# Optimization experiments

Measured on AMD Instinct MI355X. Metric: run time of the kernel, lower is better.

Reference implementation:

```python
import jax, jax.numpy as jnp
import numpy as np

N, E, F_IN, H = 100000, 500000, 1433, 32


def setup_inputs() -> dict:
    key = jax.random.key(0)
    ks = jax.random.split(key, 8)
    return {
        "x": jax.random.normal(ks[0], (N, F_IN), jnp.float32),
        "edge_index": jax.random.randint(ks[1], (2, E), 0, N, dtype=jnp.int32),
        "W1l": jax.random.normal(ks[2], (H, F_IN), jnp.float32) * 0.02,
        "b1l": jnp.zeros((H,), jnp.float32),
        "W1r": jax.random.normal(ks[3], (H, F_IN), jnp.float32) * 0.02,
        "W2l": jax.random.normal(ks[4], (H, H), jnp.float32) * 0.1,
        "b2l": jnp.zeros((H,), jnp.float32),
        "W2r": jax.random.normal(ks[5], (H, H), jnp.float32) * 0.1,
    }


def _sage_conv(x, src, tgt, Wl, bl, Wr, n_nodes):
    # PyG SAGEConv (mean aggr): out = lin_l(mean_{j->i} x_j) + lin_r(x_i)
    msg_sum = jax.ops.segment_sum(x[src], tgt, num_segments=n_nodes)  # [N, d]
    cnt = jax.ops.segment_sum(jnp.ones((src.shape[0],), x.dtype), tgt,
                              num_segments=n_nodes)                  # [N]
    agg = msg_sum / jnp.maximum(cnt, 1.0)[:, None]  # isolated nodes -> 0
    return agg @ Wl.T + bl + x @ Wr.T


def reference(x, edge_index, W1l, b1l, W1r, W2l, b2l, W2r):
    src, tgt = edge_index[0], edge_index[1]
    n = x.shape[0]
    h = _sage_conv(x, src, tgt, W1l, b1l, W1r, n)   # [N, 32]
    h = _sage_conv(h, src, tgt, W2l, b2l, W2r, n)   # [N, 32]
    h = jax.nn.relu(h)
    # dropout is identity in eval mode (training=False)
    return jax.nn.log_softmax(h, axis=1)
```

## Files before the change

### kernel.cpp

```cpp
#include <hip/hip_runtime.h>
#include <hip/hip_bf16.h>


typedef __attribute__((ext_vector_type(8))) __bf16 bf16x8;
typedef __attribute__((ext_vector_type(4))) float f32x4;

constexpr int K1 = 1433;
constexpr int KP1 = 1536;
constexpr int BK = 32;
constexpr int NS = 45;
constexpr int BM = 128;
constexpr int CONV_BLOCKS = (64 * KP1 + 64 * 32 + 255) / 256;

__device__ __forceinline__ void gload_lds16(const void* g, void* l) {
  __builtin_amdgcn_global_load_lds(
      reinterpret_cast<const __attribute__((address_space(1))) void*>(
          reinterpret_cast<uintptr_t>(g)),
      reinterpret_cast<__attribute__((address_space(3))) void*>(
          reinterpret_cast<uintptr_t>(l)),
      16, 0, 0);
}

__device__ __forceinline__ bf16x8 cvt8(const float4 lo, const float4 hi) {
  bf16x8 r;
  r[0] = (__bf16)lo.x; r[1] = (__bf16)lo.y;
  r[2] = (__bf16)lo.z; r[3] = (__bf16)lo.w;
  r[4] = (__bf16)hi.x; r[5] = (__bf16)hi.y;
  r[6] = (__bf16)hi.z; r[7] = (__bf16)hi.w;
  return r;
}

__global__ __launch_bounds__(256) void conv_zero(
    const float* __restrict__ W1l, const float* __restrict__ W1r,
    const float* __restrict__ W2l, const float* __restrict__ W2r,
    __bf16* __restrict__ wb1, __bf16* __restrict__ wb2,
    int* __restrict__ zbuf, int zcount) {
  if ((int)blockIdx.x < CONV_BLOCKS) {
    const int t = blockIdx.x * 256 + threadIdx.x;
    if (t < 64 * KP1) {
      const int c = t / KP1, k = t - c * KP1;
      float v = 0.0f;
      if (k < K1)
        v = (c < 32) ? W1l[(long)c * K1 + k] : W1r[(long)(c - 32) * K1 + k];
      wb1[t] = (__bf16)v;
    } else {
      const int u = t - 64 * KP1;
      if (u < 64 * 32) {
        const int c = u >> 5, k = u & 31;
        const float v = (c < 32) ? W2l[c * 32 + k] : W2r[(c - 32) * 32 + k];
        wb2[u] = (__bf16)v;
      }
    }
  } else {
    const int base = (blockIdx.x - CONV_BLOCKS) * 4096 + threadIdx.x * 16;
#pragma unroll
    for (int j = 0; j < 16; ++j) {
      const int i = base + j;
      if (i < zcount) zbuf[i] = 0;
    }
  }
}

__global__ __launch_bounds__(256) void gemm_big(const float* __restrict__ X,
                                                const __bf16* __restrict__ WB,
                                                __bf16* __restrict__ yl,
                                                float* __restrict__ yr,
                                                int Nrows, int gemmBlocks,
                                                const int* __restrict__ ei,
                                                int* __restrict__ deg, int E) {
  __shared__ float ldsA[2][BM][BK];
  __shared__ __bf16 ldsB[2][64][BK];
  if ((int)blockIdx.x >= gemmBlocks) {
    const int base = ((int)blockIdx.x - gemmBlocks) * 1024 + threadIdx.x;
#pragma unroll
    for (int j = 0; j < 4; ++j) {
      const int e = base + j * 256;
      if (e < E) atomicAdd(&deg[ei[E + e]], 1);
    }
    return;
  }
  const int tid = threadIdx.x;
  const int w = tid >> 6, l = tid & 63;
  const int lr = l & 15, lg = l >> 4;
  const int row0 = blockIdx.x * BM;

  const int aRowIn = (l >> 3);
  const int aChunk = (l & 7) ^ aRowIn;
  long aRow[4];
#pragma unroll
  for (int i = 0; i < 4; ++i) {
    long r = (long)row0 + w * 32 + i * 8 + aRowIn;
    if (r >= Nrows) r = Nrows - 1;
    aRow[i] = r;
  }
  const float* const pAmax = X + (size_t)Nrows * K1 - 4;
  const int bRow = w * 16 + (l >> 2);
  const int bChunk = (l & 3) ^ ((l >> 3) & 3);
  const __bf16* const pB0 = WB + (long)bRow * KP1 + bChunk * 8;

  auto stage = [&](int s, int buf) {
    const int k0 = s * BK;
#pragma unroll
    for (int i = 0; i < 4; ++i) {
      const float* g = X + aRow[i] * K1 + k0 + aChunk * 4;
      if (g > pAmax) g = pAmax;
      gload_lds16(g, &ldsA[buf][w * 32 + i * 8][0]);
    }
    gload_lds16(pB0 + k0, &ldsB[buf][w * 16][0]);
  };

  f32x4 acc[2][4];
#pragma unroll
  for (int t = 0; t < 2; ++t)
#pragma unroll
    for (int j = 0; j < 4; ++j) acc[t][j] = (f32x4){0.f, 0.f, 0.f, 0.f};

  const int swzA = lr & 7;
  const int swzB = (lr >> 1) & 3;

  stage(0, 0);
#pragma unroll 1
  for (int s = 0; s < NS; ++s) {
    const int buf = s & 1;
    if (s + 1 < NS) {
      stage(s + 1, buf ^ 1);
      asm volatile("s_waitcnt vmcnt(5)" ::: "memory");
    } else {
      asm volatile("s_waitcnt vmcnt(0)" ::: "memory");
    }
    __builtin_amdgcn_s_barrier();
    __builtin_amdgcn_sched_barrier(0);
    bf16x8 bfrag[4];
#pragma unroll
    for (int ct = 0; ct < 4; ++ct) {
      const int br = ct * 16 + lr;
      bfrag[ct] = *reinterpret_cast<const bf16x8*>(
          &ldsB[buf][br][(lg ^ swzB) * 8]);
    }
#pragma unroll
    for (int t = 0; t < 2; ++t) {
      const int fr = w * 32 + t * 16 + lr;
      const float4 u = *reinterpret_cast<const float4*>(
          &ldsA[buf][fr][((lg * 2 + 0) ^ swzA) * 4]);
      const float4 v = *reinterpret_cast<const float4*>(
          &ldsA[buf][fr][((lg * 2 + 1) ^ swzA) * 4]);
      const bf16x8 af = cvt8(u, v);
#pragma unroll
      for (int ct = 0; ct < 4; ++ct)
        acc[t][ct] =
            __builtin_amdgcn_mfma_f32_16x16x32_bf16(af, bfrag[ct], acc[t][ct], 0, 0, 0);
    }
    __builtin_amdgcn_sched_barrier(0);
    __builtin_amdgcn_s_barrier();
  }

#pragma unroll
  for (int t = 0; t < 2; ++t) {
#pragma unroll
    for (int j = 0; j < 4; ++j) {
      const long R = (long)row0 + w * 32 + t * 16 + lg * 4 + j;
      if (R < Nrows) {
#pragma unroll
        for (int ct = 0; ct < 2; ++ct)
          yl[R * 32 + ct * 16 + lr] = (__bf16)acc[t][ct][j];
#pragma unroll
        for (int ct = 2; ct < 4; ++ct)
          yr[R * 32 + (ct - 2) * 16 + lr] = acc[t][ct][j];
      }
    }
  }
}

__global__ __launch_bounds__(256) void csr_scan(const int* __restrict__ deg,
                                                int* __restrict__ tileSum,
                                                int* __restrict__ cnt,
                                                int* __restrict__ off, int n,
                                                int nT) {
  __shared__ int warpTot[4];
  __shared__ int tileOffS;
  const int b = blockIdx.x, t = threadIdx.x;
  const int base = b * 2048 + t * 8;
  int v[8];
  int s = 0;
#pragma unroll
  for (int j = 0; j < 8; ++j) {
    const int i = base + j;
    v[j] = (i < n) ? deg[i] : 0;
    s += v[j];
  }
  const int l = t & 63, w = t >> 6;
  int inc = s;
#pragma unroll
  for (int d = 1; d < 64; d <<= 1) {
    const int o = __shfl_up(inc, d);
    if (l >= d) inc += o;
  }
  if (l == 63) warpTot[w] = inc;
  __syncthreads();
  const int blockTot = warpTot[0] + warpTot[1] + warpTot[2] + warpTot[3];
  int wo = 0;
  for (int k = 0; k < w; ++k) wo += warpTot[k];
  if (t == 0) {
    __hip_atomic_store(&tileSum[b], blockTot, __ATOMIC_RELEASE,
                       __HIP_MEMORY_SCOPE_AGENT);
    atomicAdd(cnt, 1);
    while (__hip_atomic_load(cnt, __ATOMIC_ACQUIRE,
                             __HIP_MEMORY_SCOPE_AGENT) < nT) {
    }
  }
  __syncthreads();
  int tv = 0;
  if (t < 64) {
    int x2 = (t < b) ? __hip_atomic_load(&tileSum[t], __ATOMIC_ACQUIRE,
                                         __HIP_MEMORY_SCOPE_AGENT)
                     : 0;
#pragma unroll
    for (int d = 1; d < 64; d <<= 1) x2 += __shfl_xor(x2, d);
    tv = x2;
  }
  if (t == 0) tileOffS = tv;
  __syncthreads();
  int ex = tileOffS + wo + (inc - s);
#pragma unroll
  for (int j = 0; j < 8; ++j) {
    const int i = base + j;
    if (i < n) {
      off[i] = ex;
      ex += v[j];
    }
  }
}

__global__ __launch_bounds__(256) void scatter_src(const int* __restrict__ ei,
                                                   const int* __restrict__ off,
                                                   int* __restrict__ fill,
                                                   int* __restrict__ ssrc,
                                                   int E) {
  const int e = blockIdx.x * 256 + threadIdx.x;
  if (e < E) {
    const int t = ei[E + e];
    const int p = off[t] + atomicAdd(&fill[t], 1);
    ssrc[p] = ei[e];
  }
}

__global__ __launch_bounds__(256) void agg_gemm2(
    const int* __restrict__ off, const int* __restrict__ deg,
    const int* __restrict__ ssrc, const __bf16* __restrict__ yl1,
    const float* __restrict__ yr1, const float* __restrict__ b1,
    const __bf16* __restrict__ WB2, __bf16* __restrict__ yl2,
    float* __restrict__ yr2, int N) {
  __shared__ __bf16 hs[64][40];
  const int tid = threadIdx.x;
  const int nb0 = blockIdx.x * 64;
  const int c = tid & 31, r8 = tid >> 5;

  int stA[8], dgA[8];
#pragma unroll
  for (int j = 0; j < 8; ++j) {
    const int i = nb0 + r8 * 8 + j;
    stA[j] = (i < N) ? off[i] : 0;
    dgA[j] = (i < N) ? deg[i] : 0;
  }
#pragma unroll 1
  for (int j = 0; j < 8; ++j) {
    const int i = nb0 + r8 * 8 + j;
    float hv = 0.0f;
    if (i < N) {
      const int st = stA[j], d = dgA[j];
      float acc = 0.0f;
      int e = 0;
      for (; e + 4 <= d; e += 4) {
        const int s0 = ssrc[st + e + 0];
        const int s1 = ssrc[st + e + 1];
        const int s2 = ssrc[st + e + 2];
        const int s3 = ssrc[st + e + 3];
        acc += (float)yl1[(long)s0 * 32 + c] + (float)yl1[(long)s1 * 32 + c] +
               (float)yl1[(long)s2 * 32 + c] + (float)yl1[(long)s3 * 32 + c];
      }
      for (; e < d; ++e) acc += (float)yl1[(long)ssrc[st + e] * 32 + c];
      hv = acc / fmaxf((float)d, 1.0f) + b1[c] + yr1[(long)i * 32 + c];
    }
    hs[r8 * 8 + j][c] = (__bf16)hv;
  }
  __syncthreads();

  const int w = tid >> 6, l = tid & 63;
  const int lr = l & 15, lg = l >> 4;
  const bf16x8 af = *reinterpret_cast<const bf16x8*>(&hs[w * 16 + lr][lg * 8]);
  f32x4 acc4[4];
#pragma unroll
  for (int j = 0; j < 4; ++j) acc4[j] = (f32x4){0.f, 0.f, 0.f, 0.f};
#pragma unroll
  for (int ct = 0; ct < 4; ++ct) {
    const bf16x8 bf = *reinterpret_cast<const bf16x8*>(
        WB2 + (ct * 16 + lr) * 32 + lg * 8);
    acc4[ct] = __builtin_amdgcn_mfma_f32_16x16x32_bf16(af, bf, acc4[ct], 0, 0, 0);
  }
#pragma unroll
  for (int j = 0; j < 4; ++j) {
    const long R = (long)nb0 + w * 16 + lg * 4 + j;
    if (R < N) {
#pragma unroll
      for (int ct = 0; ct < 2; ++ct)
        yl2[R * 32 + ct * 16 + lr] = (__bf16)acc4[ct][j];
#pragma unroll
      for (int ct = 2; ct < 4; ++ct)
        yr2[R * 32 + (ct - 2) * 16 + lr] = acc4[ct][j];
    }
  }
}

__global__ __launch_bounds__(256) void agg_final(
    const int* __restrict__ off, const int* __restrict__ deg,
    const int* __restrict__ ssrc, const __bf16* __restrict__ yl2,
    const float* __restrict__ yr2, const float* __restrict__ bias,
    float* __restrict__ out, int N) {
  const int t = blockIdx.x * 256 + threadIdx.x;
  const int i = t >> 5, c = t & 31;
  if (i >= N) return;
  const int st = off[i], d = deg[i];
  float acc = 0.0f;
  int e = 0;
  for (; e + 4 <= d; e += 4) {
    const int s0 = ssrc[st + e + 0];
    const int s1 = ssrc[st + e + 1];
    const int s2 = ssrc[st + e + 2];
    const int s3 = ssrc[st + e + 3];
    acc += (float)yl2[(long)s0 * 32 + c] + (float)yl2[(long)s1 * 32 + c] +
           (float)yl2[(long)s2 * 32 + c] + (float)yl2[(long)s3 * 32 + c];
  }
  for (; e < d; ++e) acc += (float)yl2[(long)ssrc[st + e] * 32 + c];
  const float mean = acc / fmaxf((float)d, 1.0f);
  float v = mean + bias[c] + yr2[(long)i * 32 + c];
  v = fmaxf(v, 0.0f);
  float m = v;
#pragma unroll
  for (int dd = 16; dd >= 1; dd >>= 1) m = fmaxf(m, __shfl_xor(m, dd));
  const float ex = __expf(v - m);
  float s = ex;
#pragma unroll
  for (int dd = 16; dd >= 1; dd >>= 1) s += __shfl_xor(s, dd);
  out[(long)i * 32 + c] = (v - m) - __logf(s);
}

extern "C" void kernel_launch(void* const* d_in, const int* in_sizes, int n_in,
                              void* d_out, int out_size, void* d_ws,
                              size_t ws_size, hipStream_t stream) {
  const float* x = (const float*)d_in[0];
  const int* ei = (const int*)d_in[1];
  const float* W1l = (const float*)d_in[2];
  const float* b1l = (const float*)d_in[3];
  const float* W1r = (const float*)d_in[4];
  const float* W2l = (const float*)d_in[5];
  const float* b2l = (const float*)d_in[6];
  const float* W2r = (const float*)d_in[7];
  float* out = (float*)d_out;

  const int N = in_sizes[0] / K1;
  const int E = in_sizes[1] / 2;
  const int nTiles = (N + 2047) / 2048;

  char* ws = (char*)d_ws;
  size_t o = 0;
  auto alloc = [&](size_t bytes) {
    void* p = ws + o;
    o += (bytes + 255) & ~(size_t)255;
    return p;
  };
  __bf16* yl1 = (__bf16*)alloc((size_t)N * 32 * 2);
  float* yr1 = (float*)alloc((size_t)N * 32 * 4);
  __bf16* yl2 = (__bf16*)alloc((size_t)N * 32 * 2);
  float* yr2 = (float*)alloc((size_t)N * 32 * 4);
  __bf16* wb1 = (__bf16*)alloc((size_t)64 * KP1 * 2);
  __bf16* wb2 = (__bf16*)alloc((size_t)64 * 32 * 2);
  int* deg = (int*)alloc((size_t)(2 * N + 64) * 4);
  int* fill = deg + N;
  int* cnt = deg + 2 * N;
  int* off = (int*)alloc((size_t)N * 4);
  int* ssrc = (int*)alloc((size_t)E * 4);
  int* tileSum = (int*)alloc(64 * 4);

  const int zcount = 2 * N + 64;
  const int zBlocks = (zcount + 4095) / 4096;
  conv_zero<<<CONV_BLOCKS + zBlocks, 256, 0, stream>>>(W1l, W1r, W2l, W2r,
                                                       wb1, wb2, deg, zcount);
  const int gemmBlocks = (N + BM - 1) / BM;
  const int histBlocks = (E + 1023) / 1024;
  gemm_big<<<gemmBlocks + histBlocks, 256, 0, stream>>>(
      x, wb1, yl1, yr1, N, gemmBlocks, ei, deg, E);
  csr_scan<<<nTiles, 256, 0, stream>>>(deg, tileSum, cnt, off, N, nTiles);
  scatter_src<<<(E + 255) / 256, 256, 0, stream>>>(ei, off, fill, ssrc, E);
  agg_gemm2<<<(N + 63) / 64, 256, 0, stream>>>(off, deg, ssrc, yl1, yr1, b1l,
                                               wb2, yl2, yr2, N);
  agg_final<<<(N * 32 + 255) / 256, 256, 0, stream>>>(off, deg, ssrc, yl2,
                                                      yr2, b2l, out, N);
}
```

Before: 265.6 us.

## Fuse degree histogram, CSR scan and scatter into the big GEMM launch

Folds the edge histogram, the prefix scan over node degrees and the source scatter into role blocks at the front of the layer-1 GEMM launch. The stages are ordered by atomic counters with spin-waits, so CSR construction overlaps the dense GEMM and two kernel launches go away. The risks are deadlock or stalls if the role blocks are not all co-resident, and role blocks holding compute units the GEMM could otherwise use. Because the role blocks have the lowest block IDs they are likely dispatched first.

```diff
diff --git a/kernel.cpp b/kernel.cpp
--- a/kernel.cpp
+++ b/kernel.cpp
@@ -11,6 +11,8 @@
 constexpr int NS = 45;
 constexpr int BM = 128;
 constexpr int CONV_BLOCKS = (64 * KP1 + 64 * 32 + 255) / 256;
+constexpr int HIST_BLOCKS = 192;
+constexpr int SCAT_BLOCKS = 128;
 
 __device__ __forceinline__ void gload_lds16(const void* g, void* l) {
   __builtin_amdgcn_global_load_lds(
@@ -61,28 +63,113 @@
   }
 }
 
-__global__ __launch_bounds__(256) void gemm_big(const float* __restrict__ X,
-                                                const __bf16* __restrict__ WB,
-                                                __bf16* __restrict__ yl,
-                                                float* __restrict__ yr,
-                                                int Nrows, int gemmBlocks,
-                                                const int* __restrict__ ei,
-                                                int* __restrict__ deg, int E) {
+__global__ __launch_bounds__(256) void gemm_fused(
+    const float* __restrict__ X, const __bf16* __restrict__ WB,
+    __bf16* __restrict__ yl, float* __restrict__ yr, int Nrows,
+    const int* __restrict__ ei, int* __restrict__ deg, int E,
+    int* __restrict__ off, int* __restrict__ fill, int* __restrict__ ssrc,
+    int* __restrict__ tileSum, int* __restrict__ cnts, int nT) {
   __shared__ float ldsA[2][BM][BK];
   __shared__ __bf16 ldsB[2][64][BK];
-  if ((int)blockIdx.x >= gemmBlocks) {
-    const int base = ((int)blockIdx.x - gemmBlocks) * 1024 + threadIdx.x;
-#pragma unroll
-    for (int j = 0; j < 4; ++j) {
-      const int e = base + j * 256;
-      if (e < E) atomicAdd(&deg[ei[E + e]], 1);
-    }
+  __shared__ int warpTot[4];
+  __shared__ int tileOffS;
+  const int bid = blockIdx.x;
+  const int tid = threadIdx.x;
+  const int roleEnd = HIST_BLOCKS + nT + SCAT_BLOCKS;
+
+  if (bid < HIST_BLOCKS) {
+    for (int e = bid * 256 + tid; e < E; e += HIST_BLOCKS * 256)
+      atomicAdd(&deg[ei[E + e]], 1);
+    __threadfence();
+    __syncthreads();
+    if (tid == 0) atomicAdd(&cnts[0], 1);
     return;
   }
-  const int tid = threadIdx.x;
+  if (bid < HIST_BLOCKS + nT) {
+    const int b = bid - HIST_BLOCKS;
+    if (tid == 0) {
+      while (__hip_atomic_load(&cnts[0], __ATOMIC_ACQUIRE,
+                               __HIP_MEMORY_SCOPE_AGENT) < HIST_BLOCKS) {
+        __builtin_amdgcn_s_sleep(2);
+      }
+    }
+    __syncthreads();
+    const int base = b * 2048 + tid * 8;
+    int v[8];
+    int s = 0;
+#pragma unroll
+    for (int j = 0; j < 8; ++j) {
+      const int i = base + j;
+      v[j] = (i < Nrows) ? deg[i] : 0;
+      s += v[j];
+    }
+    const int l = tid & 63, w = tid >> 6;
+    int inc = s;
+#pragma unroll
+    for (int d = 1; d < 64; d <<= 1) {
+      const int o = __shfl_up(inc, d);
+      if (l >= d) inc += o;
+    }
+    if (l == 63) warpTot[w] = inc;
+    __syncthreads();
+    const int blockTot = warpTot[0] + warpTot[1] + warpTot[2] + warpTot[3];
+    int wo = 0;
+    for (int k = 0; k < w; ++k) wo += warpTot[k];
+    if (tid == 0) {
+      __hip_atomic_store(&tileSum[b], blockTot, __ATOMIC_RELEASE,
+                         __HIP_MEMORY_SCOPE_AGENT);
+      atomicAdd(&cnts[1], 1);
+      while (__hip_atomic_load(&cnts[1], __ATOMIC_ACQUIRE,
+                               __HIP_MEMORY_SCOPE_AGENT) < nT) {
+        __builtin_amdgcn_s_sleep(2);
+      }
+    }
+    __syncthreads();
+    int tv = 0;
+    if (tid < 64) {
+      int x2 = (tid < b) ? __hip_atomic_load(&tileSum[tid], __ATOMIC_ACQUIRE,
+                                             __HIP_MEMORY_SCOPE_AGENT)
+                         : 0;
+#pragma unroll
+      for (int d = 1; d < 64; d <<= 1) x2 += __shfl_xor(x2, d);
+      tv = x2;
+    }
+    if (tid == 0) tileOffS = tv;
+    __syncthreads();
+    int ex = tileOffS + wo + (inc - s);
+#pragma unroll
+    for (int j = 0; j < 8; ++j) {
+      const int i = base + j;
+      if (i < Nrows) {
+        off[i] = ex;
+        ex += v[j];
+      }
+    }
+    __threadfence();
+    __syncthreads();
+    if (tid == 0) atomicAdd(&cnts[2], 1);
+    return;
+  }
+  if (bid < roleEnd) {
+    if (tid == 0) {
+      while (__hip_atomic_load(&cnts[2], __ATOMIC_ACQUIRE,
+                               __HIP_MEMORY_SCOPE_AGENT) < nT) {
+        __builtin_amdgcn_s_sleep(2);
+      }
+    }
+    __syncthreads();
+    const int sb = bid - HIST_BLOCKS - nT;
+    for (int e = sb * 256 + tid; e < E; e += SCAT_BLOCKS * 256) {
+      const int t = ei[E + e];
+      const int p = off[t] + atomicAdd(&fill[t], 1);
+      ssrc[p] = ei[e];
+    }
+    return;
+  }
+
   const int w = tid >> 6, l = tid & 63;
   const int lr = l & 15, lg = l >> 4;
-  const int row0 = blockIdx.x * BM;
+  const int row0 = (bid - roleEnd) * BM;
 
   const int aRowIn = (l >> 3);
   const int aChunk = (l & 7) ^ aRowIn;
@@ -168,79 +255,6 @@
           yr[R * 32 + (ct - 2) * 16 + lr] = acc[t][ct][j];
       }
     }
-  }
-}
-
-__global__ __launch_bounds__(256) void csr_scan(const int* __restrict__ deg,
-                                                int* __restrict__ tileSum,
-                                                int* __restrict__ cnt,
-                                                int* __restrict__ off, int n,
-                                                int nT) {
-  __shared__ int warpTot[4];
-  __shared__ int tileOffS;
-  const int b = blockIdx.x, t = threadIdx.x;
-  const int base = b * 2048 + t * 8;
-  int v[8];
-  int s = 0;
-#pragma unroll
-  for (int j = 0; j < 8; ++j) {
-    const int i = base + j;
-    v[j] = (i < n) ? deg[i] : 0;
-    s += v[j];
-  }
-  const int l = t & 63, w = t >> 6;
-  int inc = s;
-#pragma unroll
-  for (int d = 1; d < 64; d <<= 1) {
-    const int o = __shfl_up(inc, d);
-    if (l >= d) inc += o;
-  }
-  if (l == 63) warpTot[w] = inc;
-  __syncthreads();
-  const int blockTot = warpTot[0] + warpTot[1] + warpTot[2] + warpTot[3];
-  int wo = 0;
-  for (int k = 0; k < w; ++k) wo += warpTot[k];
-  if (t == 0) {
-    __hip_atomic_store(&tileSum[b], blockTot, __ATOMIC_RELEASE,
-                       __HIP_MEMORY_SCOPE_AGENT);
-    atomicAdd(cnt, 1);
-    while (__hip_atomic_load(cnt, __ATOMIC_ACQUIRE,
-                             __HIP_MEMORY_SCOPE_AGENT) < nT) {
-    }
-  }
-  __syncthreads();
-  int tv = 0;
-  if (t < 64) {
-    int x2 = (t < b) ? __hip_atomic_load(&tileSum[t], __ATOMIC_ACQUIRE,
-                                         __HIP_MEMORY_SCOPE_AGENT)
-                     : 0;
-#pragma unroll
-    for (int d = 1; d < 64; d <<= 1) x2 += __shfl_xor(x2, d);
-    tv = x2;
-  }
-  if (t == 0) tileOffS = tv;
-  __syncthreads();
-  int ex = tileOffS + wo + (inc - s);
-#pragma unroll
-  for (int j = 0; j < 8; ++j) {
-    const int i = base + j;
-    if (i < n) {
-      off[i] = ex;
-      ex += v[j];
-    }
-  }
-}
-
-__global__ __launch_bounds__(256) void scatter_src(const int* __restrict__ ei,
-                                                   const int* __restrict__ off,
-                                                   int* __restrict__ fill,
-                                                   int* __restrict__ ssrc,
-                                                   int E) {
-  const int e = blockIdx.x * 256 + threadIdx.x;
-  if (e < E) {
-    const int t = ei[E + e];
-    const int p = off[t] + atomicAdd(&fill[t], 1);
-    ssrc[p] = ei[e];
   }
 }
 
@@ -376,7 +390,7 @@
   __bf16* wb2 = (__bf16*)alloc((size_t)64 * 32 * 2);
   int* deg = (int*)alloc((size_t)(2 * N + 64) * 4);
   int* fill = deg + N;
-  int* cnt = deg + 2 * N;
+  int* cnts = deg + 2 * N;
   int* off = (int*)alloc((size_t)N * 4);
   int* ssrc = (int*)alloc((size_t)E * 4);
   int* tileSum = (int*)alloc(64 * 4);
@@ -386,11 +400,10 @@
   conv_zero<<<CONV_BLOCKS + zBlocks, 256, 0, stream>>>(W1l, W1r, W2l, W2r,
                                                        wb1, wb2, deg, zcount);
   const int gemmBlocks = (N + BM - 1) / BM;
-  const int histBlocks = (E + 1023) / 1024;
-  gemm_big<<<gemmBlocks + histBlocks, 256, 0, stream>>>(
-      x, wb1, yl1, yr1, N, gemmBlocks, ei, deg, E);
-  csr_scan<<<nTiles, 256, 0, stream>>>(deg, tileSum, cnt, off, N, nTiles);
-  scatter_src<<<(E + 255) / 256, 256, 0, stream>>>(ei, off, fill, ssrc, E);
+  const int roleBlocks = HIST_BLOCKS + nTiles + SCAT_BLOCKS;
+  gemm_fused<<<roleBlocks + gemmBlocks, 256, 0, stream>>>(
+      x, wb1, yl1, yr1, N, ei, deg, E, off, fill, ssrc, tileSum, cnts,
+      nTiles);
   agg_gemm2<<<(N + 63) / 64, 256, 0, stream>>>(off, deg, ssrc, yl1, yr1, b1l,
                                                wb2, yl2, yr2, N);
   agg_final<<<(N * 32 + 255) / 256, 256, 0, stream>>>(off, deg, ssrc, yl2,
```

Result: slower. 337.1 us (+26.9%).
